# Performance work log

Measured on AMD Instinct MI355X. Metric: run time of the kernel, lower is better.

Reference implementation:

```python
import jax, jax.numpy as jnp
import numpy as np

NEG_INF = -1e9  # matches tf mask value -1000000000.0
LEAKY_ALPHA = 0.2  # tf.nn.leaky_relu default


def setup_inputs() -> dict:
    key = jax.random.key(0)
    k1, k2, k3, k4 = jax.random.split(key, 4)
    B, N, F, U = 8, 2048, 128, 128
    X = jax.random.normal(k1, (B, N, F), dtype=jnp.float32)
    A = jax.random.randint(k2, (B, N, N), 0, 2, dtype=jnp.int32)
    W = jax.random.normal(k3, (F, U), dtype=jnp.float32) * 0.1
    a = jax.random.normal(k4, (2 * U, 1), dtype=jnp.float32) * 0.1
    return {"X": X, "A": A, "W": W, "a": a}


def reference(X, A, W, a):
    # H = X @ W : [B, N, U]
    H = jnp.einsum('bnf,fu->bnu', X, W)
    U = H.shape[-1]
    # Additive decomposition of the tile+concat: [H_i || H_j] @ a = H_i@a_src + H_j@a_dst
    a_src = a[:U, 0]   # [U]
    a_dst = a[U:, 0]   # [U]
    s = H @ a_src      # [B, N]
    t = H @ a_dst      # [B, N]
    e = s[:, :, None] + t[:, None, :]            # [B, N, N] pairwise logits
    e = jax.nn.leaky_relu(e, negative_slope=LEAKY_ALPHA)
    mask = jnp.where(A > 0, 0.0, NEG_INF).astype(e.dtype)
    attention = jax.nn.softmax(e + mask, axis=-1)  # [B, N, N]
    H_out = jnp.einsum('bij,bju->biu', attention, H)
    return jax.nn.relu(H_out)
```

## Files before the change

kernel.cpp:

```cpp
#include <hip/hip_runtime.h>
#include <hip/hip_bf16.h>


#define NEG_INF -1.0e9f

typedef __bf16 bf16x8 __attribute__((ext_vector_type(8)));
typedef unsigned short ushort8 __attribute__((ext_vector_type(8)));
typedef float f32x4 __attribute__((ext_vector_type(4)));

__device__ __forceinline__ unsigned short f2b(float x) {
    unsigned u = __builtin_bit_cast(unsigned, x);
    u += 0x7fffu + ((u >> 16) & 1u);
    return (unsigned short)(u >> 16);
}

__device__ __forceinline__ void gload_lds16(const void* g, void* l) {
    __builtin_amdgcn_global_load_lds(
        (const __attribute__((address_space(1))) void*)g,
        (__attribute__((address_space(3))) void*)l, 16, 0, 0);
}

__global__ __launch_bounds__(256) void k_wt(const float* __restrict__ W,
                                            unsigned short* __restrict__ WT) {
    int tid = blockIdx.x * 256 + threadIdx.x;
    int u = tid >> 7, f = tid & 127;
    WT[tid] = f2b(W[f * 128 + u]);
}

__global__ __launch_bounds__(256) void k_h(const float* __restrict__ X,
                                           const unsigned short* __restrict__ WT,
                                           const float* __restrict__ a,
                                           unsigned short* __restrict__ HT,
                                           float* __restrict__ sbuf,
                                           float* __restrict__ tbuf) {
    const int tid  = threadIdx.x;
    const int w    = tid >> 6;
    const int lane = tid & 63;
    const int r    = lane & 15;
    const int cg   = lane >> 4;
    const int row0 = blockIdx.x * 64 + w * 16;
    const int b    = row0 >> 11;
    const int n0   = row0 & 2047;
    const int arow = row0 + r;

    f32x4 acc[8] = {};

#pragma unroll
    for (int k0 = 0; k0 < 128; k0 += 32) {
        const float* xp = X + (size_t)arow * 128 + k0 + cg * 8;
        ushort8 xa;
#pragma unroll
        for (int j = 0; j < 8; j++) xa[j] = f2b(xp[j]);
        bf16x8 av = __builtin_bit_cast(bf16x8, xa);
#pragma unroll
        for (int ut = 0; ut < 8; ut++) {
            ushort8 wb = *(const ushort8*)(WT + (size_t)(ut * 16 + r) * 128 + k0 + cg * 8);
            acc[ut] = __builtin_amdgcn_mfma_f32_16x16x32_bf16(
                av, __builtin_bit_cast(bf16x8, wb), acc[ut], 0, 0, 0);
        }
    }

    float sp[4] = {0.f, 0.f, 0.f, 0.f};
    float tp[4] = {0.f, 0.f, 0.f, 0.f};
#pragma unroll
    for (int ut = 0; ut < 8; ut++) {
        int u = ut * 16 + r;
        float as = a[u];
        float ad = a[128 + u];
#pragma unroll
        for (int reg = 0; reg < 4; reg++) {
            float h = acc[ut][reg];
            int nrow = n0 + cg * 4 + reg;
            HT[((size_t)b * 128 + u) * 2048 + nrow] = f2b(h);
            sp[reg] += h * as;
            tp[reg] += h * ad;
        }
    }
#pragma unroll
    for (int msk = 1; msk < 16; msk <<= 1) {
#pragma unroll
        for (int reg = 0; reg < 4; reg++) {
            sp[reg] += __shfl_xor(sp[reg], msk);
            tp[reg] += __shfl_xor(tp[reg], msk);
        }
    }
    if (r == 0) {
#pragma unroll
        for (int reg = 0; reg < 4; reg++) {
            int row = row0 + cg * 4 + reg;
            sbuf[row] = sp[reg];
            tbuf[row] = tp[reg];
        }
    }
}

__global__ __launch_bounds__(512, 4) void k_attn(const int* __restrict__ A,
                                                 const unsigned short* __restrict__ HT,
                                                 const float* __restrict__ sbuf,
                                                 const float* __restrict__ tbuf,
                                                 float* __restrict__ out) {
    __shared__ char smem[65536];
    __shared__ float tS[2048];
    __shared__ float dSm[4][2][16];

    const int tid  = threadIdx.x;
    const int w    = tid >> 6;
    const int lane = tid & 63;
    const int r    = lane & 15;
    const int cg   = lane >> 4;
    const int g    = w & 1;
    const int jq   = w >> 1;
    const int bid  = blockIdx.x;
    const int b    = bid & 7;
    const int it   = bid >> 3;
    const int i0   = it * 32;
    const int rot  = it & 15;

    const int irow = i0 + g * 16 + r;
    const float s_r = sbuf[b * 2048 + irow];
    const unsigned short* Hb = HT + ((size_t)b * 128) * 2048 + jq * 512;
    const int* Aq = A + ((size_t)(b * 2048 + irow)) * 2048 + jq * 512 + cg * 8;

    const int srow = (lane >> 2);
    const int csrc = (lane & 3) ^ ((lane >> 2) & 3) ^ ((lane >> 4) & 3);
    char* const qbase = smem + jq * 16384;
    const unsigned short* src0 = Hb + (size_t)(g * 64 + srow) * 2048 + csrc * 8;
    const int rsl = ((r & 3) ^ ((r >> 2) & 3));

    f32x4 acc[8] = {};
    float den = 0.f;

    *(float4*)(tS + tid * 4) = *(const float4*)(tbuf + b * 2048 + tid * 4);

    int4 aP[2][2];
    {
        const int j0 = rot * 32;
        const int j1 = ((1 + rot) & 15) * 32;
        aP[0][0] = *(const int4*)(Aq + j0);
        aP[0][1] = *(const int4*)(Aq + j0 + 4);
        aP[1][0] = *(const int4*)(Aq + j1);
        aP[1][1] = *(const int4*)(Aq + j1 + 4);
#pragma unroll
        for (int i = 0; i < 4; i++)
            gload_lds16(src0 + (size_t)i * 16 * 2048 + j0,
                        qbase + (g * 4 + i) * 1024);
    }
    __syncthreads();

#pragma unroll
    for (int k = 0; k < 16; ++k) {
        const int p = k & 1;

        const float* tq = tS + jq * 512 + ((k + rot) & 15) * 32 + cg * 8;
        float4 t0 = *(const float4*)(tq);
        float4 t1 = *(const float4*)(tq + 4);
        float tv[8] = {t0.x, t0.y, t0.z, t0.w, t1.x, t1.y, t1.z, t1.w};
        int4 ca = aP[k & 1][0], cb = aP[k & 1][1];
        int ai[8] = {ca.x, ca.y, ca.z, ca.w, cb.x, cb.y, cb.z, cb.w};
        bf16x8 pa;
#pragma unroll
        for (int jj = 0; jj < 8; jj++) {
            float x = s_r + tv[jj];
            float e = fmaxf(x, 0.2f * x);
            float pp = __expf(e - 16.0f);
            pp = ai[jj] > 0 ? pp : 0.f;
            den += pp;
            pa[jj] = (__bf16)pp;
        }

        if (k < 14) {
            const int ja = ((k + 2 + rot) & 15) * 32;
            aP[k & 1][0] = *(const int4*)(Aq + ja);
            aP[k & 1][1] = *(const int4*)(Aq + ja + 4);
        }
        if (k < 15) {
            const int jn = ((k + 1 + rot) & 15) * 32;
            char* dst = qbase + (p ^ 1) * 8192;
#pragma unroll
            for (int i = 0; i < 4; i++)
                gload_lds16(src0 + (size_t)i * 16 * 2048 + jn * 1,
                            dst + (g * 4 + i) * 1024);
        }

        if (k < 14)      asm volatile("s_waitcnt vmcnt(6)" ::: "memory");
        else if (k < 15) asm volatile("s_waitcnt vmcnt(4)" ::: "memory");
        else             asm volatile("s_waitcnt vmcnt(0)" ::: "memory");
        __builtin_amdgcn_s_barrier();
        __builtin_amdgcn_sched_barrier(0);

        const char* buf = qbase + p * 8192;
#pragma unroll
        for (int ut = 0; ut < 8; ut++) {
            ushort8 hb = *(const ushort8*)(buf + (ut * 16 + r) * 64 +
                                           ((cg ^ rsl) * 16));
            acc[ut] = __builtin_amdgcn_mfma_f32_16x16x32_bf16(
                pa, __builtin_bit_cast(bf16x8, hb), acc[ut], 0, 0, 0);
        }

        __builtin_amdgcn_s_barrier();
        __builtin_amdgcn_sched_barrier(0);
    }

    den += __shfl_xor(den, 16);
    den += __shfl_xor(den, 32);

    float* accS = (float*)smem;
    if (cg == 0) dSm[jq][g][r] = den;
    if (jq != 0) {
        const int rowIdx = ((jq - 1) * 2 + g) * 16 + cg * 4;
#pragma unroll
        for (int ut = 0; ut < 8; ut++)
#pragma unroll
            for (int reg = 0; reg < 4; reg++)
                accS[(rowIdx + reg) * 132 + ut * 16 + r] = acc[ut][reg];
    }
    __syncthreads();
    if (jq == 0) {
        float dinv[4];
#pragma unroll
        for (int reg = 0; reg < 4; reg++) {
            const int row = cg * 4 + reg;
            dinv[reg] = 1.0f / (dSm[0][g][row] + dSm[1][g][row] +
                                dSm[2][g][row] + dSm[3][g][row]);
        }
#pragma unroll
        for (int ut = 0; ut < 8; ut++) {
#pragma unroll
            for (int reg = 0; reg < 4; reg++) {
                const int lrow = cg * 4 + reg;
                float num = acc[ut][reg]
                          + accS[((0 * 2 + g) * 16 + lrow) * 132 + ut * 16 + r]
                          + accS[((1 * 2 + g) * 16 + lrow) * 132 + ut * 16 + r]
                          + accS[((2 * 2 + g) * 16 + lrow) * 132 + ut * 16 + r];
                float o = fmaxf(num * dinv[reg], 0.f);
                out[((size_t)(b * 2048 + i0 + g * 16 + lrow)) * 128 +
                    ut * 16 + r] = o;
            }
        }
    }
}

extern "C" void kernel_launch(void* const* d_in, const int* in_sizes, int n_in,
                              void* d_out, int out_size, void* d_ws, size_t ws_size,
                              hipStream_t stream) {
    const float* X = (const float*)d_in[0];
    const int*   A = (const int*)d_in[1];
    const float* W = (const float*)d_in[2];
    const float* a = (const float*)d_in[3];
    float* out = (float*)d_out;

    char* ws = (char*)d_ws;
    unsigned short* WT  = (unsigned short*)(ws);
    float*          sb  = (float*)(ws + 32768);
    float*          tb  = (float*)(ws + 98304);
    unsigned short* HT  = (unsigned short*)(ws + 163840);

    k_wt<<<dim3(64), dim3(256), 0, stream>>>(W, WT);
    k_h<<<dim3(256), dim3(256), 0, stream>>>(X, WT, a, HT, sb, tb);
    k_attn<<<dim3(512), dim3(512), 0, stream>>>(A, HT, sb, tb, out);
}
```

Baseline: 59.64 us.

## Fuse W transpose into k_h and prefetch t values from global in attention

Removes the separate W-transpose kernel: each k_h block now converts and transposes W into padded shared memory itself, saving a launch but redoing the transpose in every block. In the attention kernel the shared-memory staging of tbuf is replaced by per-thread register prefetch of t alongside the A mask loads, two steps ahead. Loads are now issued before the exp computation so they overlap it, and the waitcnt values are adjusted to match. The trailing barrier on the last iteration is replaced by a __syncthreads before the reduction, and shared memory use drops slightly.

```diff
diff --git a/kernel.cpp b/kernel.cpp
--- a/kernel.cpp
+++ b/kernel.cpp
@@ -20,24 +20,26 @@
         (__attribute__((address_space(3))) void*)l, 16, 0, 0);
 }
 
-__global__ __launch_bounds__(256) void k_wt(const float* __restrict__ W,
-                                            unsigned short* __restrict__ WT) {
-    int tid = blockIdx.x * 256 + threadIdx.x;
-    int u = tid >> 7, f = tid & 127;
-    WT[tid] = f2b(W[f * 128 + u]);
-}
-
 __global__ __launch_bounds__(256) void k_h(const float* __restrict__ X,
-                                           const unsigned short* __restrict__ WT,
+                                           const float* __restrict__ W,
                                            const float* __restrict__ a,
                                            unsigned short* __restrict__ HT,
                                            float* __restrict__ sbuf,
                                            float* __restrict__ tbuf) {
+    __shared__ unsigned short WT[128 * 136];
+
     const int tid  = threadIdx.x;
     const int w    = tid >> 6;
     const int lane = tid & 63;
     const int r    = lane & 15;
     const int cg   = lane >> 4;
+
+    for (int i = tid; i < 16384; i += 256) {
+        int u = i >> 7, f = i & 127;
+        WT[u * 136 + f] = f2b(W[f * 128 + u]);
+    }
+    __syncthreads();
+
     const int row0 = blockIdx.x * 64 + w * 16;
     const int b    = row0 >> 11;
     const int n0   = row0 & 2047;
@@ -54,7 +56,7 @@
         bf16x8 av = __builtin_bit_cast(bf16x8, xa);
 #pragma unroll
         for (int ut = 0; ut < 8; ut++) {
-            ushort8 wb = *(const ushort8*)(WT + (size_t)(ut * 16 + r) * 128 + k0 + cg * 8);
+            ushort8 wb = *(const ushort8*)(&WT[(ut * 16 + r) * 136 + k0 + cg * 8]);
             acc[ut] = __builtin_amdgcn_mfma_f32_16x16x32_bf16(
                 av, __builtin_bit_cast(bf16x8, wb), acc[ut], 0, 0, 0);
         }
@@ -100,7 +102,6 @@
                                                  const float* __restrict__ tbuf,
                                                  float* __restrict__ out) {
     __shared__ char smem[65536];
-    __shared__ float tS[2048];
     __shared__ float dSm[4][2][16];
 
     const int tid  = threadIdx.x;
@@ -119,7 +120,8 @@
     const int irow = i0 + g * 16 + r;
     const float s_r = sbuf[b * 2048 + irow];
     const unsigned short* Hb = HT + ((size_t)b * 128) * 2048 + jq * 512;
-    const int* Aq = A + ((size_t)(b * 2048 + irow)) * 2048 + jq * 512 + cg * 8;
+    const int*   Aq = A    + ((size_t)(b * 2048 + irow)) * 2048 + jq * 512 + cg * 8;
+    const float* Tq = tbuf + (size_t)b * 2048 + jq * 512 + cg * 8;
 
     const int srow = (lane >> 2);
     const int csrc = (lane & 3) ^ ((lane >> 2) & 3) ^ ((lane >> 4) & 3);
@@ -130,16 +132,19 @@
     f32x4 acc[8] = {};
     float den = 0.f;
 
-    *(float4*)(tS + tid * 4) = *(const float4*)(tbuf + b * 2048 + tid * 4);
-
-    int4 aP[2][2];
+    int4   aP[2][2];
+    float4 tP[2][2];
     {
         const int j0 = rot * 32;
         const int j1 = ((1 + rot) & 15) * 32;
         aP[0][0] = *(const int4*)(Aq + j0);
         aP[0][1] = *(const int4*)(Aq + j0 + 4);
+        tP[0][0] = *(const float4*)(Tq + j0);
+        tP[0][1] = *(const float4*)(Tq + j0 + 4);
         aP[1][0] = *(const int4*)(Aq + j1);
         aP[1][1] = *(const int4*)(Aq + j1 + 4);
+        tP[1][0] = *(const float4*)(Tq + j1);
+        tP[1][1] = *(const float4*)(Tq + j1 + 4);
 #pragma unroll
         for (int i = 0; i < 4; i++)
             gload_lds16(src0 + (size_t)i * 16 * 2048 + j0,
@@ -151,12 +156,27 @@
     for (int k = 0; k < 16; ++k) {
         const int p = k & 1;
 
-        const float* tq = tS + jq * 512 + ((k + rot) & 15) * 32 + cg * 8;
-        float4 t0 = *(const float4*)(tq);
-        float4 t1 = *(const float4*)(tq + 4);
-        float tv[8] = {t0.x, t0.y, t0.z, t0.w, t1.x, t1.y, t1.z, t1.w};
-        int4 ca = aP[k & 1][0], cb = aP[k & 1][1];
-        int ai[8] = {ca.x, ca.y, ca.z, ca.w, cb.x, cb.y, cb.z, cb.w};
+        int4   ca = aP[p][0],  cb = aP[p][1];
+        float4 ct0 = tP[p][0], ct1 = tP[p][1];
+
+        if (k < 15) {
+            const int jn = ((k + 1 + rot) & 15) * 32;
+            char* dst = qbase + (p ^ 1) * 8192;
+#pragma unroll
+            for (int i = 0; i < 4; i++)
+                gload_lds16(src0 + (size_t)i * 16 * 2048 + jn,
+                            dst + (g * 4 + i) * 1024);
+        }
+        if (k < 14) {
+            const int ja = ((k + 2 + rot) & 15) * 32;
+            aP[p][0] = *(const int4*)(Aq + ja);
+            aP[p][1] = *(const int4*)(Aq + ja + 4);
+            tP[p][0] = *(const float4*)(Tq + ja);
+            tP[p][1] = *(const float4*)(Tq + ja + 4);
+        }
+
+        float tv[8] = {ct0.x, ct0.y, ct0.z, ct0.w, ct1.x, ct1.y, ct1.z, ct1.w};
+        int   ai[8] = {ca.x, ca.y, ca.z, ca.w, cb.x, cb.y, cb.z, cb.w};
         bf16x8 pa;
 #pragma unroll
         for (int jj = 0; jj < 8; jj++) {
@@ -168,21 +188,7 @@
             pa[jj] = (__bf16)pp;
         }
 
-        if (k < 14) {
-            const int ja = ((k + 2 + rot) & 15) * 32;
-            aP[k & 1][0] = *(const int4*)(Aq + ja);
-            aP[k & 1][1] = *(const int4*)(Aq + ja + 4);
-        }
-        if (k < 15) {
-            const int jn = ((k + 1 + rot) & 15) * 32;
-            char* dst = qbase + (p ^ 1) * 8192;
-#pragma unroll
-            for (int i = 0; i < 4; i++)
-                gload_lds16(src0 + (size_t)i * 16 * 2048 + jn * 1,
-                            dst + (g * 4 + i) * 1024);
-        }
-
-        if (k < 14)      asm volatile("s_waitcnt vmcnt(6)" ::: "memory");
+        if (k < 14)      asm volatile("s_waitcnt vmcnt(8)" ::: "memory");
         else if (k < 15) asm volatile("s_waitcnt vmcnt(4)" ::: "memory");
         else             asm volatile("s_waitcnt vmcnt(0)" ::: "memory");
         __builtin_amdgcn_s_barrier();
@@ -197,12 +203,16 @@
                 pa, __builtin_bit_cast(bf16x8, hb), acc[ut], 0, 0, 0);
         }
 
-        __builtin_amdgcn_s_barrier();
-        __builtin_amdgcn_sched_barrier(0);
+        if (k < 15) {
+            __builtin_amdgcn_s_barrier();
+            __builtin_amdgcn_sched_barrier(0);
+        }
     }
 
     den += __shfl_xor(den, 16);
     den += __shfl_xor(den, 32);
+
+    __syncthreads();
 
     float* accS = (float*)smem;
     if (cg == 0) dSm[jq][g][r] = den;
@@ -250,12 +260,10 @@
     float* out = (float*)d_out;
 
     char* ws = (char*)d_ws;
-    unsigned short* WT  = (unsigned short*)(ws);
-    float*          sb  = (float*)(ws + 32768);
-    float*          tb  = (float*)(ws + 98304);
-    unsigned short* HT  = (unsigned short*)(ws + 163840);
-
-    k_wt<<<dim3(64), dim3(256), 0, stream>>>(W, WT);
-    k_h<<<dim3(256), dim3(256), 0, stream>>>(X, WT, a, HT, sb, tb);
+    float*          sb  = (float*)(ws);
+    float*          tb  = (float*)(ws + 65536);
+    unsigned short* HT  = (unsigned short*)(ws + 131072);
+
+    k_h<<<dim3(256), dim3(256), 0, stream>>>(X, W, a, HT, sb, tb);
     k_attn<<<dim3(512), dim3(512), 0, stream>>>(A, HT, sb, tb, out);
 }
```

Result: slower. 61.96 us (+3.9%).
